# Kernel tuning notes

Hardware: AMD Instinct MI355X
Metric: run time of the kernel (lower is better)

The kernel has to match this reference:

```python
import jax, jax.numpy as jnp
import numpy as np

B, S, H, E, V, NSTEPS = 8, 128, 512, 512, 32000, 8


def setup_inputs() -> dict:
    key = jax.random.key(0)
    ks = jax.random.split(key, 24)

    def lin(k, fi, fo):
        return (jax.random.normal(k, (fi, fo), jnp.float32) / np.sqrt(fi).astype(np.float32))

    return {
        "input_ids": jax.random.randint(ks[0], (B, S), 0, V),
        "tree_ids": jax.random.randint(ks[1], (B, NSTEPS, 3, S), 0, S),
        "emb": jax.random.normal(ks[2], (V, E), jnp.float32) * 0.02,
        "W_ioux": lin(ks[3], E, 3 * H),
        "W_iouh_r": lin(ks[4], H, 3 * H),
        "b_iouh_r": jnp.zeros((3 * H,), jnp.float32),
        "W_iouh_l": lin(ks[5], H, 3 * H),
        "b_iouh_l": jnp.zeros((3 * H,), jnp.float32),
        "W_fx": lin(ks[6], E, H),
        "W_fh0": lin(ks[7], H, H),
        "b_fh0": jnp.zeros((H,), jnp.float32),
        "W_fh1": lin(ks[8], H, H),
        "b_fh1": jnp.zeros((H,), jnp.float32),
        "W_fh2": lin(ks[9], H, H),
        "b_fh2": jnp.zeros((H,), jnp.float32),
        "W_fh3": lin(ks[10], H, H),
        "b_fh3": jnp.zeros((H,), jnp.float32),
    }


def _scatter_rows(vals, idx):
    # out[b, idx[b, j], k] += vals[b, j, k]  (torch scatter_add_ along dim 1)
    return jax.vmap(lambda v, i: jnp.zeros_like(v).at[i].add(v))(vals, idx)


def _gather_rows(vals, idx):
    # out[b, j, k] = vals[b, idx[b, j], k]  (torch gather along dim 1)
    return jnp.take_along_axis(vals, idx[:, :, None], axis=1)


def _masked_scatter(dest, mask_rows, src):
    # Exact torch masked_scatter_ semantics: flatten mask/src, fill True slots
    # with consecutive elements of flattened src.
    m = jnp.broadcast_to(mask_rows[:, :, None], dest.shape).reshape(-1)
    pos = jnp.clip(jnp.cumsum(m) - 1, 0, None)
    out = jnp.where(m, src.reshape(-1)[pos], dest.reshape(-1))
    return out.reshape(dest.shape)


def reference(input_ids, tree_ids, emb, W_ioux, W_iouh_r, b_iouh_r, W_iouh_l,
              b_iouh_l, W_fx, W_fh0, b_fh0, W_fh1, b_fh1, W_fh2, b_fh2,
              W_fh3, b_fh3):
    x = emb[input_ids]                      # [B, S, E]
    Hs = W_fx.shape[1]
    iou_x = x @ W_ioux                      # [B, S, 3H], loop-invariant
    fx_x = x @ W_fx                         # [B, S, H],  loop-invariant
    h0 = jnp.zeros(x.shape[:2] + (Hs,), x.dtype)
    c0 = jnp.zeros_like(h0)
    steps = jnp.transpose(tree_ids, (1, 0, 2, 3))  # [n_steps, B, 3, S]

    def step(carry, t):
        h, c = carry
        idx_d, idx_r, idx_l = t[:, 0], t[:, 1], t[:, 2]
        iou_hr = h @ W_iouh_r + b_iouh_r
        iou_hl = h @ W_iouh_l + b_iouh_l
        # torch scatter_add_ with an index of width H into a 3H buffer only
        # touches the first H channels -- replicate that exactly.
        scat = _scatter_rows(iou_hr[..., :Hs], idx_r) + _scatter_rows(iou_hl[..., :Hs], idx_l)
        iou = iou_x.at[..., :Hs].add(scat)
        i, o, u = jnp.split(iou, 3, axis=-1)
        i, o, u = jax.nn.sigmoid(i), jax.nn.sigmoid(o), jnp.tanh(u)
        # fh0 and fh1 share idx_r, fh2 and fh3 share idx_l -> fold linearly.
        fh_r = h @ (W_fh0 + W_fh1) + (b_fh0 + b_fh1)
        fh_l = h @ (W_fh2 + W_fh3) + (b_fh2 + b_fh3)
        f = jax.nn.sigmoid(_gather_rows(fx_x, idx_d)
                           + _gather_rows(fh_r, idx_r)
                           + _gather_rows(fh_l, idx_l))
        fc = f * c
        c_full = i * u + _scatter_rows(fc, idx_d)
        h_full = o * jnp.tanh(c_full)
        mask = idx_d != 0
        h_new = _masked_scatter(h, mask, h_full)
        c_new = _masked_scatter(c, mask, c_full)
        return (h_new, c_new), None

    (h, c), _ = jax.lax.scan(step, (h0, c0), steps)
    return h
```

## Files before the change

### kernel.cpp

```cpp
#include <hip/hip_runtime.h>
#include <hip/hip_bf16.h>

#define B_ 8
#define S_ 128
#define H_ 512
#define E_ 512
#define NST 8
#define R_ 1024
#define N2 2048
#define KD 512
#define LDA 72
#define NBLK 512
#define GRP 64

typedef __hip_bfloat16 bf16;
typedef __attribute__((ext_vector_type(8))) short v8s;
typedef __attribute__((ext_vector_type(4))) float v4f;
typedef unsigned long long u64;

__device__ __forceinline__ float sigm(float x){ return 1.0f/(1.0f + expf(-x)); }
__device__ __forceinline__ float load_in(const void* p, long long i, int isb){
    return isb ? __bfloat162float(((const bf16*)p)[i]) : ((const float*)p)[i];
}
__device__ __forceinline__ int idx_read(const int* p, int j, int is64){
    return is64 ? p[2*j] : p[j];
}
__device__ __forceinline__ unsigned short f2b(float v){
    bf16 b = __float2bfloat16(v);
    return *(unsigned short*)&b;
}

__device__ __forceinline__ float vload1f(const float* p){
    return __hip_atomic_load(p, __ATOMIC_RELAXED, __HIP_MEMORY_SCOPE_AGENT);
}
__device__ __forceinline__ void vstore1(float* p, float v){
    __hip_atomic_store(p, v, __ATOMIC_RELAXED, __HIP_MEMORY_SCOPE_AGENT);
}
__device__ __forceinline__ void vstore_hb2(unsigned short* p, unsigned short a, unsigned short b){
    unsigned int u = (unsigned)a | ((unsigned)b << 16);
    __hip_atomic_store((unsigned int*)p, u, __ATOMIC_RELAXED, __HIP_MEMORY_SCOPE_AGENT);
}
__device__ __forceinline__ v8s vload16(const unsigned short* p){
    union { u64 u[2]; v8s v; } c;
    c.u[0] = __hip_atomic_load((const u64*)p,     __ATOMIC_RELAXED, __HIP_MEMORY_SCOPE_AGENT);
    c.u[1] = __hip_atomic_load(((const u64*)p)+1, __ATOMIC_RELAXED, __HIP_MEMORY_SCOPE_AGENT);
    return c.v;
}

__device__ __forceinline__ void gsync(int* bar, int gen){
    __syncthreads();
    if (threadIdx.x == 0){
        int g = blockIdx.x >> 6;
        int* ga = bar + 64*(1+g);
        int* gd = bar + 64*(9+g);
        int old = __hip_atomic_fetch_add(ga, 1, __ATOMIC_RELAXED, __HIP_MEMORY_SCOPE_AGENT);
        if (old + 1 == GRP*gen){
            __hip_atomic_fetch_add(bar, GRP, __ATOMIC_RELAXED, __HIP_MEMORY_SCOPE_AGENT);
            while (__hip_atomic_load(bar, __ATOMIC_RELAXED, __HIP_MEMORY_SCOPE_AGENT) < NBLK*gen)
                __builtin_amdgcn_s_sleep(4);
            __hip_atomic_fetch_add(gd, 1, __ATOMIC_RELAXED, __HIP_MEMORY_SCOPE_AGENT);
        } else {
            while (__hip_atomic_load(gd, __ATOMIC_RELAXED, __HIP_MEMORY_SCOPE_AGENT) < gen)
                __builtin_amdgcn_s_sleep(4);
        }
    }
    __syncthreads();
}

__global__ void probe_all(const void* t0, const void* t1, const void* t2, const void* t3,
                          const void* t4, const void* t5, const void* t6, const void* t7,
                          const void* t8, const void* t9, const void* t10, const void* t11,
                          const void* t12, const void* t13, const void* t14,
                          const int* __restrict__ ids, const int* __restrict__ tree,
                          int* __restrict__ flags){
    const void* ts[15] = {t0,t1,t2,t3,t4,t5,t6,t7,t8,t9,t10,t11,t12,t13,t14};
    int bid = blockIdx.x, t = threadIdx.x;
    int bad = 0;
    if (bid < 15){
        if (t < 512){
            unsigned short u = ((const unsigned short*)ts[bid])[t];
            bad = (((u >> 7) & 0xFF) >= 140);
        }
    } else {
        const int* p = (bid == 15) ? ids : tree;
        int n = (bid == 15) ? 1024 : 2048;
        for (int j = t; j < n; j += 1024)
            if (j & 1) bad |= (p[j] != 0);
    }
    unsigned long long bl = __ballot(bad);
    __shared__ int acc[16];
    if ((t & 63) == 0) acc[t >> 6] = (bl != 0ull) ? 1 : 0;
    __syncthreads();
    if (t == 0){
        int any = 0;
        for (int w = 0; w < 16; ++w) any |= acc[w];
        flags[(bid < 15) ? bid : (16 + bid - 15)] = any ? 0 : 1;
    }
}

#define NB2 320
#define GS2 (NB2*512)
__global__ __launch_bounds__(512)
void rank_pack(const void* __restrict__ Wioux, const void* __restrict__ Wfx,
               const void* __restrict__ Wr, const void* __restrict__ Wl,
               const void* __restrict__ W0, const void* __restrict__ W1,
               const void* __restrict__ W2, const void* __restrict__ W3,
               const void* __restrict__ br, const void* __restrict__ bl,
               const void* __restrict__ b0, const void* __restrict__ b1,
               const void* __restrict__ b2, const void* __restrict__ b3,
               const int* __restrict__ ids, const void* __restrict__ emb,
               const int* __restrict__ tree,
               unsigned short* __restrict__ WxT, unsigned short* __restrict__ WcatT,
               float* __restrict__ bcat, unsigned short* __restrict__ xb,
               float* __restrict__ h0,
               int* __restrict__ msk, int* __restrict__ rnk, int* __restrict__ cnt,
               const int* __restrict__ flags, int* __restrict__ bar){
    int bid = blockIdx.x, tid = threadIdx.x;
    int is64 = flags[17];
    if (bid == 0){
        for (int i = tid; i < 64*17; i += 512) bar[i] = 0;
    }
    if (bid < 8){
        int st = bid;
        for (int c = tid; c < R_; c += 512){
            cnt[(0*NST + st)*R_ + c] = 0;
            cnt[(1*NST + st)*R_ + c] = 0;
            cnt[(2*NST + st)*R_ + c] = 0;
        }
        __syncthreads();
        __shared__ int wt[8];
        int runbase = 0;
        for (int ch = 0; ch < 2; ++ch){
            int t = ch*512 + tid;
            int b = t >> 7, s = t & 127;
            int base = (b*NST + st)*3*S_;
            int d0 = idx_read(tree, base + s, is64);
            int rd = (b<<7) + d0;
            int rr = (b<<7) + idx_read(tree, base + S_ + s, is64);
            int rl = (b<<7) + idx_read(tree, base + 2*S_ + s, is64);
            int m = (d0 != 0) ? 1 : 0;
            unsigned long long bal = __ballot(m);
            int lane = tid & 63, wv = tid >> 6;
            if (lane == 0) wt[wv] = __popcll(bal);
            __syncthreads();
            int bp = runbase, tot = 0;
            for (int w = 0; w < wv; ++w) bp += wt[w];
            for (int w = 0; w < 8; ++w) tot += wt[w];
            int rank = bp + __popcll(bal & ((1ull << lane) - 1ull));
            msk[st*R_ + t] = m;
            rnk[st*R_ + t] = m ? rank : 0;
            atomicAdd(&cnt[(0*NST + st)*R_ + rr], 1);
            atomicAdd(&cnt[(1*NST + st)*R_ + rl], 1);
            atomicAdd(&cnt[(2*NST + st)*R_ + rd], 1);
            runbase += tot;
            __syncthreads();
        }
    }
    int gt = bid*512 + tid;
    {
        int f_wx = flags[1], f_wf = flags[6];
        for (int u = gt; u < 131072; u += GS2){
            int n = u >> 6, k0 = (u & 63)*8;
            unsigned short tmp[8];
            #pragma unroll
            for (int i = 0; i < 8; ++i){
                float v = (n < 1536) ? load_in(Wioux, (long long)(k0+i)*1536 + n, f_wx)
                                     : load_in(Wfx,   (long long)(k0+i)*512 + (n-1536), f_wf);
                tmp[i] = f2b(v);
            }
            *(v8s*)&WxT[(size_t)n*KD + k0] = *(v8s*)tmp;
        }
    }
    {
        int fWr=flags[2], fWl=flags[4], fW0=flags[7], fW1=flags[9], fW2=flags[11], fW3=flags[13];
        for (int u = gt; u < 131072; u += GS2){
            int n = u >> 6, k0 = (u & 63)*8;
            unsigned short tmp[8];
            #pragma unroll
            for (int i = 0; i < 8; ++i){
                long long k = k0 + i;
                float v;
                if      (n <  512) v = load_in(Wr, k*1536 + n, fWr);
                else if (n < 1024) v = load_in(Wl, k*1536 + (n-512), fWl);
                else if (n < 1536) { int c = n-1024; v = load_in(W0, k*512+c, fW0) + load_in(W1, k*512+c, fW1); }
                else               { int c = n-1536; v = load_in(W2, k*512+c, fW2) + load_in(W3, k*512+c, fW3); }
                tmp[i] = f2b(v);
            }
            *(v8s*)&WcatT[(size_t)n*KD + k0] = *(v8s*)tmp;
        }
    }
    {
        int fbr=flags[3], fbl=flags[5], fb0=flags[8], fb1=flags[10], fb2=flags[12], fb3=flags[14];
        for (int n = gt; n < 2048; n += GS2){
            float v;
            if      (n <  512) v = load_in(br, n, fbr);
            else if (n < 1024) v = load_in(bl, n-512, fbl);
            else if (n < 1536) v = load_in(b0, n-1024, fb0) + load_in(b1, n-1024, fb1);
            else               v = load_in(b2, n-1536, fb2) + load_in(b3, n-1536, fb3);
            bcat[n] = v;
        }
    }
    {
        int f_emb = flags[0], i64i = flags[16];
        for (int u = gt; u < 65536; u += GS2){
            int r = u >> 6, c0 = (u & 63)*8;
            long long base = (long long)idx_read(ids, r, i64i)*E_ + c0;
            unsigned short tmp[8];
            #pragma unroll
            for (int i = 0; i < 8; ++i) tmp[i] = f2b(load_in(emb, base + i, f_emb));
            *(v8s*)&xb[(size_t)r*KD + c0] = *(v8s*)tmp;
        }
    }
    for (int u = gt; u < 262144; u += GS2)
        ((float4*)h0)[u] = make_float4(0.f,0.f,0.f,0.f);
}

__global__ void csr_scan(const int* __restrict__ cnt, int* __restrict__ off,
                         int* __restrict__ cur){
    int st = blockIdx.x, a = blockIdx.y;
    int t = threadIdx.x;
    int base = (a*NST + st)*R_;
    __shared__ int sh[R_];
    int v = cnt[base + t];
    sh[t] = v;
    __syncthreads();
    for (int d = 1; d < R_; d <<= 1){
        int x = (t >= d) ? sh[t - d] : 0;
        __syncthreads();
        sh[t] += x;
        __syncthreads();
    }
    int excl = sh[t] - v;
    off[base + t] = excl;
    cur[base + t] = excl;
}

__global__ __launch_bounds__(512)
void csr_fill(const int* __restrict__ tree, int* __restrict__ cur,
              int* __restrict__ ent, const int* __restrict__ flags){
    int is64 = flags[17];
    int st = blockIdx.x;
    for (int ch = 0; ch < 2; ++ch){
        int t = ch*512 + threadIdx.x;
        int b = t >> 7, s = t & 127;
        int base = (b*NST + st)*3*S_;
        int rd = (b<<7) + idx_read(tree, base + s, is64);
        int rr = (b<<7) + idx_read(tree, base + S_ + s, is64);
        int rl = (b<<7) + idx_read(tree, base + 2*S_ + s, is64);
        int p0 = atomicAdd(&cur[(0*NST + st)*R_ + rr], 1);
        ent[(0*NST + st)*R_ + p0] = t;
        int p1 = atomicAdd(&cur[(1*NST + st)*R_ + rl], 1);
        ent[(1*NST + st)*R_ + p1] = t;
        int p2 = atomicAdd(&cur[(2*NST + st)*R_ + rd], 1);
        ent[(2*NST + st)*R_ + p2] = t | (rr << 10) | (rl << 20);
    }
}

__device__ __forceinline__ void gemm_phase(const unsigned short* __restrict__ A,
               const unsigned short* __restrict__ BT,
               const float* __restrict__ bias,
               float* __restrict__ C,
               short* __restrict__ SMEM)
{
    int bid = blockIdx.x;
    int bn = (bid & 7)*4 + ((bid >> 3) & 3);
    int bm = bid >> 5;
    int tid = threadIdx.x;
    int lane = tid & 63, wave = tid >> 6;
    int grp = wave >> 2, w4 = wave & 3;
    int wm = w4 & 1, wn = w4 >> 1;
    int lm = lane & 15, quad = lane >> 4;
    short* As = SMEM + grp*(2*64*LDA);
    short* Bs = As + 64*LDA;
    v4f acc[2][2];
    #pragma unroll
    for (int i=0;i<2;++i)
        #pragma unroll
        for (int j=0;j<2;++j) acc[i][j] = (v4f)0.0f;

    int t = tid & 255;
    int srow = t >> 3, sg = (t & 7)*8;
    int kb = grp*256;
    const unsigned short* Ab = A  + (size_t)(bm*64)*KD + kb;
    const unsigned short* Bb = BT + (size_t)(bn*64)*KD + kb;
    v8s pa[2], pb[2];
    #pragma unroll
    for (int j=0;j<2;++j){
        pa[j] = vload16(Ab + (size_t)(j*32+srow)*KD + sg);
        pb[j] = *(const v8s*)(Bb + (size_t)(j*32+srow)*KD + sg);
    }
    for (int k0 = 0; k0 < 256; k0 += 64){
        #pragma unroll
        for (int j=0;j<2;++j){
            *(v8s*)&As[(j*32+srow)*LDA + sg] = pa[j];
            *(v8s*)&Bs[(j*32+srow)*LDA + sg] = pb[j];
        }
        __syncthreads();
        int k1 = k0 + 64;
        if (k1 < 256){
            #pragma unroll
            for (int j=0;j<2;++j){
                pa[j] = vload16(Ab + (size_t)(j*32+srow)*KD + k1 + sg);
                pb[j] = *(const v8s*)(Bb + (size_t)(j*32+srow)*KD + k1 + sg);
            }
        }
        #pragma unroll
        for (int kk = 0; kk < 64; kk += 32){
            v8s af[2], bf[2];
            #pragma unroll
            for (int i=0;i<2;++i){
                af[i] = *(const v8s*)&As[(wm*32 + i*16 + lm)*LDA + kk + quad*8];
                bf[i] = *(const v8s*)&Bs[(wn*32 + i*16 + lm)*LDA + kk + quad*8];
            }
            #pragma unroll
            for (int i=0;i<2;++i)
                #pragma unroll
                for (int j=0;j<2;++j)
                    acc[i][j] = __builtin_amdgcn_mfma_f32_16x16x32_bf16(af[i], bf[j], acc[i][j], 0, 0, 0);
        }
        __syncthreads();
    }
    float* Red = (float*)SMEM;
    if (grp){
        #pragma unroll
        for (int i=0;i<2;++i)
            #pragma unroll
            for (int j=0;j<2;++j)
                #pragma unroll
                for (int rg=0;rg<4;++rg)
                    Red[(wm*32 + i*16 + quad*4 + rg)*64 + (wn*32 + j*16 + lm)] = acc[i][j][rg];
    }
    __syncthreads();
    if (!grp){
        #pragma unroll
        for (int j=0;j<2;++j){
            int n = bn*64 + wn*32 + j*16 + lm;
            float bv = bias ? bias[n] : 0.0f;
            #pragma unroll
            for (int i=0;i<2;++i){
                int m0 = bm*64 + wm*32 + i*16 + quad*4;
                #pragma unroll
                for (int rg = 0; rg < 4; ++rg){
                    float v = acc[i][j][rg] + Red[(wm*32 + i*16 + quad*4 + rg)*64 + (wn*32 + j*16 + lm)] + bv;
                    vstore1(&C[(size_t)(m0+rg)*N2 + n], v);
                }
            }
        }
    }
}

__device__ __forceinline__ void epi_phase(const float* __restrict__ XO,
              const float* __restrict__ T, int tstr,
              const float* __restrict__ hc, const float* __restrict__ cc,
              float* __restrict__ hn, float* __restrict__ cn,
              unsigned short* __restrict__ hb, float* __restrict__ out,
              const int* __restrict__ msk, const int* __restrict__ rnk,
              const int* __restrict__ cnt, const int* __restrict__ off,
              const int* __restrict__ ent, int st, int last)
{
    int c = threadIdx.x;
    #pragma unroll
    for (int rr2 = 0; rr2 < 2; ++rr2){
        int r = blockIdx.x*2 + rr2;
        if (!msk[st*R_ + r]){
            float hv = vload1f(&hc[(size_t)r*H_ + c]);
            if (last){
                out[(size_t)r*H_ + c] = hv;
            } else {
                vstore1(&hn[(size_t)r*H_ + c], hv);
                vstore1(&cn[(size_t)r*H_ + c], vload1f(&cc[(size_t)r*H_ + c]));
                unsigned v16 = f2b(hv);
                unsigned o16 = __shfl_down((int)v16, 1);
                if (!(c & 1)) vstore_hb2(&hb[(size_t)r*KD + c], (unsigned short)v16, (unsigned short)o16);
            }
            continue;
        }
        int j = rnk[st*R_ + r];
        int bR = off[(0*NST+st)*R_ + j], dR = cnt[(0*NST+st)*R_ + j];
        int bL = off[(1*NST+st)*R_ + j], dL = cnt[(1*NST+st)*R_ + j];
        int bD = off[(2*NST+st)*R_ + j], dD = cnt[(2*NST+st)*R_ + j];
        const int* eR = ent + (0*NST+st)*R_ + bR;
        const int* eL = ent + (1*NST+st)*R_ + bL;
        const int* eD = ent + (2*NST+st)*R_ + bD;
        const float* xo = XO + (size_t)j*N2;
        float scv = 0.f;
        {
            int e = 0;
            for (; e + 4 <= dR; e += 4){
                int a0=eR[e], a1=eR[e+1], a2=eR[e+2], a3=eR[e+3];
                float t0 = vload1f(&T[(size_t)a0*tstr + c]);
                float t1 = vload1f(&T[(size_t)a1*tstr + c]);
                float t2 = vload1f(&T[(size_t)a2*tstr + c]);
                float t3 = vload1f(&T[(size_t)a3*tstr + c]);
                scv += (t0 + t1) + (t2 + t3);
            }
            for (; e < dR; ++e) scv += vload1f(&T[(size_t)eR[e]*tstr + c]);
        }
        {
            int e = 0;
            for (; e + 4 <= dL; e += 4){
                int a0=eL[e], a1=eL[e+1], a2=eL[e+2], a3=eL[e+3];
                float t0 = vload1f(&T[(size_t)a0*tstr + 512 + c]);
                float t1 = vload1f(&T[(size_t)a1*tstr + 512 + c]);
                float t2 = vload1f(&T[(size_t)a2*tstr + 512 + c]);
                float t3 = vload1f(&T[(size_t)a3*tstr + 512 + c]);
                scv += (t0 + t1) + (t2 + t3);
            }
            for (; e < dL; ++e) scv += vload1f(&T[(size_t)eL[e]*tstr + 512 + c]);
        }
        float fxv = vload1f(&xo[1536 + c]);
        float csc = 0.f;
        {
            int e = 0;
            for (; e + 2 <= dD; e += 2){
                int p0 = eD[e], p1 = eD[e+1];
                int s0 = p0 & 1023, ra0 = (p0 >> 10) & 1023, rb0 = (p0 >> 20) & 1023;
                int s1 = p1 & 1023, ra1 = (p1 >> 10) & 1023, rb1 = (p1 >> 20) & 1023;
                float ta0 = vload1f(&T[(size_t)ra0*tstr + 1024 + c]);
                float tb0 = vload1f(&T[(size_t)rb0*tstr + 1536 + c]);
                float cv0 = vload1f(&cc[(size_t)s0*H_ + c]);
                float ta1 = vload1f(&T[(size_t)ra1*tstr + 1024 + c]);
                float tb1 = vload1f(&T[(size_t)rb1*tstr + 1536 + c]);
                float cv1 = vload1f(&cc[(size_t)s1*H_ + c]);
                csc += sigm(fxv + ta0 + tb0) * cv0 + sigm(fxv + ta1 + tb1) * cv1;
            }
            for (; e < dD; ++e){
                int pk = eD[e];
                int s  = pk & 1023, ra = (pk >> 10) & 1023, rb = (pk >> 20) & 1023;
                float ta = vload1f(&T[(size_t)ra*tstr + 1024 + c]);
                float tb = vload1f(&T[(size_t)rb*tstr + 1536 + c]);
                float cv = vload1f(&cc[(size_t)s*H_ + c]);
                csc += sigm(fxv + ta + tb) * cv;
            }
        }
        float ig = sigm(vload1f(&xo[c]) + scv);
        float og = sigm(vload1f(&xo[512 + c]));
        float ug = tanhf(vload1f(&xo[1024 + c]));
        float cf = ig*ug + csc;
        float hf = og * tanhf(cf);
        if (last){
            out[(size_t)r*H_ + c] = hf;
        } else {
            vstore1(&hn[(size_t)r*H_ + c], hf);
            vstore1(&cn[(size_t)r*H_ + c], cf);
            unsigned v16 = f2b(hf);
            unsigned o16 = __shfl_down((int)v16, 1);
            if (!(c & 1)) vstore_hb2(&hb[(size_t)r*KD + c], (unsigned short)v16, (unsigned short)o16);
        }
    }
}

__global__ __launch_bounds__(512, 4)
void chain_all(const unsigned short* __restrict__ xb,
               const unsigned short* __restrict__ WxT,
               const unsigned short* __restrict__ WcatT,
               const float* __restrict__ bcat,
               float* __restrict__ XO, float* __restrict__ T,
               float* __restrict__ h0, float* __restrict__ c0,
               float* __restrict__ h1, float* __restrict__ c1,
               unsigned short* __restrict__ hb, float* __restrict__ out,
               const int* __restrict__ msk, const int* __restrict__ rnk,
               const int* __restrict__ cnt, const int* __restrict__ off,
               const int* __restrict__ ent, int* bar)
{
    __shared__ short SMEM[4*64*LDA];
    int gen = 0;

    gemm_phase(xb, WxT, (const float*)nullptr, XO, SMEM);
    gsync(bar, ++gen);
    epi_phase(XO, bcat, 0, h0, c0, h1, c1, hb, out, msk, rnk, cnt, off, ent, 0, 0);
    gsync(bar, ++gen);

    for (int st = 1; st < NST; ++st){
        const float* hcp = (st & 1) ? h1 : h0;
        const float* ccp = (st & 1) ? c1 : c0;
        float* hnp = (st & 1) ? h0 : h1;
        float* cnp = (st & 1) ? c0 : c1;
        gemm_phase(hb, WcatT, bcat, T, SMEM);
        gsync(bar, ++gen);
        epi_phase(XO, T, N2, hcp, ccp, hnp, cnp, hb, out,
                  msk, rnk, cnt, off, ent, st, (st == NST-1) ? 1 : 0);
        if (st < NST-1) gsync(bar, ++gen);
    }
}

extern "C" void kernel_launch(void* const* d_in, const int* in_sizes, int n_in,
                              void* d_out, int out_size, void* d_ws, size_t ws_size,
                              hipStream_t stream) {
    const int* input_ids = (const int*)d_in[0];
    const int* tree      = (const int*)d_in[1];

    char* wp = (char*)d_ws;
    auto alloc = [&](size_t bytes) -> void* {
        void* q = (void*)wp;
        wp += (bytes + 255) & ~(size_t)255;
        return q;
    };
    float*          XO     = (float*)alloc((size_t)R_*N2*4);
    float*          T      = (float*)alloc((size_t)R_*N2*4);
    float*          h0     = (float*)alloc((size_t)R_*H_*4);
    float*          c0     = (float*)alloc((size_t)R_*H_*4);
    float*          h1     = (float*)alloc((size_t)R_*H_*4);
    float*          c1     = (float*)alloc((size_t)R_*H_*4);
    unsigned short* WxT    = (unsigned short*)alloc((size_t)N2*KD*2);
    unsigned short* WcatT  = (unsigned short*)alloc((size_t)N2*KD*2);
    float*          bcat   = (float*)alloc((size_t)N2*4);
    unsigned short* xb     = (unsigned short*)alloc((size_t)R_*KD*2);
    unsigned short* hb     = (unsigned short*)alloc((size_t)R_*KD*2);
    int*            msk    = (int*)alloc((size_t)NST*R_*4);
    int*            rnk    = (int*)alloc((size_t)NST*R_*4);
    int*            cnt    = (int*)alloc((size_t)3*NST*R_*4);
    int*            off    = (int*)alloc((size_t)3*NST*R_*4);
    int*            cur    = (int*)alloc((size_t)3*NST*R_*4);
    int*            ent    = (int*)alloc((size_t)3*NST*R_*4);
    int*            flags  = (int*)alloc(256);
    int*            bar    = (int*)alloc(8192);
    float*          out    = (float*)d_out;

    hipLaunchKernelGGL(probe_all, dim3(17), dim3(1024), 0, stream,
                       d_in[2], d_in[3], d_in[4], d_in[5], d_in[6], d_in[7], d_in[8],
                       d_in[9], d_in[10], d_in[11], d_in[12], d_in[13], d_in[14],
                       d_in[15], d_in[16], input_ids, tree, flags);
    hipLaunchKernelGGL(rank_pack, dim3(NB2), dim3(512), 0, stream,
                       d_in[3], d_in[8],
                       d_in[4], d_in[6], d_in[9], d_in[11], d_in[13], d_in[15],
                       d_in[5], d_in[7], d_in[10], d_in[12], d_in[14], d_in[16],
                       input_ids, d_in[2], tree,
                       WxT, WcatT, bcat, xb, h0, msk, rnk, cnt, flags, bar);
    hipLaunchKernelGGL(csr_scan, dim3(NST, 3), dim3(1024), 0, stream, cnt, off, cur);
    hipLaunchKernelGGL(csr_fill, dim3(NST), dim3(512), 0, stream, tree, cur, ent, flags);

    hipLaunchKernelGGL(chain_all, dim3(NBLK), dim3(512), 0, stream,
                       xb, WxT, WcatT, bcat, XO, T, h0, c0, h1, c1, hb, out,
                       msk, rnk, cnt, off, ent, bar);
}
```

Measured before the change: 295.5 us.

## Replace post-GEMM grid barrier with per-group dependency counters and prefetch A tiles

Replaces the full grid barrier between each GEMM phase and its epilogue with per-group arrival counters. Each block waits only on the row groups its epilogue rows depend on, found through mask and rank. The GEMM A-operand chunks are all loaded into registers up front instead of double-buffered, and the barrier sleep interval is shortened. This cuts global synchronisation latency, but relies on the dependency analysis being complete (epilogue gathers through CSR entries may touch other groups) and raises register pressure.

```diff
diff --git a/kernel.cpp b/kernel.cpp
--- a/kernel.cpp
+++ b/kernel.cpp
@@ -57,11 +57,11 @@
         if (old + 1 == GRP*gen){
             __hip_atomic_fetch_add(bar, GRP, __ATOMIC_RELAXED, __HIP_MEMORY_SCOPE_AGENT);
             while (__hip_atomic_load(bar, __ATOMIC_RELAXED, __HIP_MEMORY_SCOPE_AGENT) < NBLK*gen)
-                __builtin_amdgcn_s_sleep(4);
+                __builtin_amdgcn_s_sleep(2);
             __hip_atomic_fetch_add(gd, 1, __ATOMIC_RELAXED, __HIP_MEMORY_SCOPE_AGENT);
         } else {
             while (__hip_atomic_load(gd, __ATOMIC_RELAXED, __HIP_MEMORY_SCOPE_AGENT) < gen)
-                __builtin_amdgcn_s_sleep(4);
+                __builtin_amdgcn_s_sleep(2);
         }
     }
     __syncthreads();
@@ -118,7 +118,7 @@
     int bid = blockIdx.x, tid = threadIdx.x;
     int is64 = flags[17];
     if (bid == 0){
-        for (int i = tid; i < 64*17; i += 512) bar[i] = 0;
+        for (int i = tid; i < 64*81; i += 512) bar[i] = 0;
     }
     if (bid < 8){
         int st = bid;
@@ -283,26 +283,27 @@
     int kb = grp*256;
     const unsigned short* Ab = A  + (size_t)(bm*64)*KD + kb;
     const unsigned short* Bb = BT + (size_t)(bn*64)*KD + kb;
-    v8s pa[2], pb[2];
+    v8s pa[4][2], pb[2];
     #pragma unroll
-    for (int j=0;j<2;++j){
-        pa[j] = vload16(Ab + (size_t)(j*32+srow)*KD + sg);
+    for (int q=0;q<4;++q)
+        #pragma unroll
+        for (int j=0;j<2;++j)
+            pa[q][j] = vload16(Ab + (size_t)(j*32+srow)*KD + q*64 + sg);
+    #pragma unroll
+    for (int j=0;j<2;++j)
         pb[j] = *(const v8s*)(Bb + (size_t)(j*32+srow)*KD + sg);
-    }
-    for (int k0 = 0; k0 < 256; k0 += 64){
+    #pragma unroll
+    for (int q = 0; q < 4; ++q){
         #pragma unroll
         for (int j=0;j<2;++j){
-            *(v8s*)&As[(j*32+srow)*LDA + sg] = pa[j];
+            *(v8s*)&As[(j*32+srow)*LDA + sg] = pa[q][j];
             *(v8s*)&Bs[(j*32+srow)*LDA + sg] = pb[j];
         }
         __syncthreads();
-        int k1 = k0 + 64;
-        if (k1 < 256){
-            #pragma unroll
-            for (int j=0;j<2;++j){
-                pa[j] = vload16(Ab + (size_t)(j*32+srow)*KD + k1 + sg);
-                pb[j] = *(const v8s*)(Bb + (size_t)(j*32+srow)*KD + k1 + sg);
-            }
+        if (q < 3){
+            #pragma unroll
+            for (int j=0;j<2;++j)
+                pb[j] = *(const v8s*)(Bb + (size_t)(j*32+srow)*KD + (q+1)*64 + sg);
         }
         #pragma unroll
         for (int kk = 0; kk < 64; kk += 32){
@@ -356,12 +357,12 @@
               unsigned short* __restrict__ hb, float* __restrict__ out,
               const int* __restrict__ msk, const int* __restrict__ rnk,
               const int* __restrict__ cnt, const int* __restrict__ off,
-              const int* __restrict__ ent, int st, int last)
+              const int* __restrict__ ent, int st, int last, int r0)
 {
     int c = threadIdx.x;
     #pragma unroll
     for (int rr2 = 0; rr2 < 2; ++rr2){
-        int r = blockIdx.x*2 + rr2;
+        int r = r0 + rr2;
         if (!msk[st*R_ + r]){
             float hv = vload1f(&hc[(size_t)r*H_ + c]);
             if (last){
@@ -464,11 +465,38 @@
                const int* __restrict__ ent, int* bar)
 {
     __shared__ short SMEM[4*64*LDA];
+    int bid = blockIdx.x;
+    int bG  = bid >> 6;
+    int r0  = (bG << 7) + ((bid & 63) << 1);
+    int* sc = bar + 64*17;
     int gen = 0;
 
+    auto sig = [&](int st){
+        __syncthreads();
+        if (threadIdx.x == 0)
+            __hip_atomic_fetch_add(sc + 64*(st*8 + bG), 1,
+                                   __ATOMIC_RELAXED, __HIP_MEMORY_SCOPE_AGENT);
+    };
+    auto waitc = [&](int st, int b){
+        int* p = sc + 64*(st*8 + b);
+        while (__hip_atomic_load(p, __ATOMIC_RELAXED, __HIP_MEMORY_SCOPE_AGENT) < 64)
+            __builtin_amdgcn_s_sleep(1);
+    };
+
     gemm_phase(xb, WxT, (const float*)nullptr, XO, SMEM);
-    gsync(bar, ++gen);
-    epi_phase(XO, bcat, 0, h0, c0, h1, c1, hb, out, msk, rnk, cnt, off, ent, 0, 0);
+    sig(0);
+    {
+        int m0 = msk[r0], m1 = msk[r0 + 1];
+        int jb0 = m0 ? (rnk[r0] >> 7) : bG;
+        int jb1 = m1 ? (rnk[r0 + 1] >> 7) : bG;
+        if (threadIdx.x == 0){
+            waitc(0, jb0);
+            if (jb1 != jb0) waitc(0, jb1);
+        }
+        __syncthreads();
+        epi_phase(XO, bcat, 0, h0, c0, h1, c1, hb, out,
+                  msk, rnk, cnt, off, ent, 0, 0, r0);
+    }
     gsync(bar, ++gen);
 
     for (int st = 1; st < NST; ++st){
@@ -477,9 +505,20 @@
         float* hnp = (st & 1) ? h0 : h1;
         float* cnp = (st & 1) ? c0 : c1;
         gemm_phase(hb, WcatT, bcat, T, SMEM);
-        gsync(bar, ++gen);
-        epi_phase(XO, T, N2, hcp, ccp, hnp, cnp, hb, out,
-                  msk, rnk, cnt, off, ent, st, (st == NST-1) ? 1 : 0);
+        sig(st);
+        {
+            int m0 = msk[st*R_ + r0], m1 = msk[st*R_ + r0 + 1];
+            int jb0 = m0 ? (rnk[st*R_ + r0] >> 7) : bG;
+            int jb1 = m1 ? (rnk[st*R_ + r0 + 1] >> 7) : bG;
+            if (threadIdx.x == 0){
+                waitc(st, bG);
+                if (jb0 != bG) waitc(st, jb0);
+                if (jb1 != bG && jb1 != jb0) waitc(st, jb1);
+            }
+            __syncthreads();
+            epi_phase(XO, T, N2, hcp, ccp, hnp, cnp, hb, out,
+                      msk, rnk, cnt, off, ent, st, (st == NST-1) ? 1 : 0, r0);
+        }
         if (st < NST-1) gsync(bar, ++gen);
     }
 }
@@ -514,7 +553,7 @@
     int*            cur    = (int*)alloc((size_t)3*NST*R_*4);
     int*            ent    = (int*)alloc((size_t)3*NST*R_*4);
     int*            flags  = (int*)alloc(256);
-    int*            bar    = (int*)alloc(8192);
+    int*            bar    = (int*)alloc(32768);
     float*          out    = (float*)d_out;
 
     hipLaunchKernelGGL(probe_all, dim3(17), dim3(1024), 0, stream,
```

After: 324.6 us. 9.8% more time.
